# Performance work log

Hardware: AMD Instinct MI355X
Metric: run time of the kernel (lower is better)

Reference implementation:

```python
import jax, jax.numpy as jnp
import numpy as np

L, B, T, E, NH, HD, HID, V = 8, 2, 2048, 1024, 16, 64, 2816, 32000


def _rmsnorm(x, w, eps=1e-6):
    return w * (x * jax.lax.rsqrt(jnp.mean(x * x, axis=-1, keepdims=True) + eps))


def _rope(x, cos, sin):
    # x: [B,H,T,D]; cos/sin: [1,1,T,D/2]
    x1, x2 = jnp.split(x, 2, axis=-1)
    return jnp.concatenate([x1 * cos - x2 * sin, x1 * sin + x2 * cos], axis=-1)


def setup_inputs() -> dict:
    key = jax.random.key(0)
    ks = jax.random.split(key, 7)
    s = 0.02
    return {
        "idx": jax.random.randint(ks[0], (B, T), 0, V),
        "tok_emb": jax.random.normal(ks[1], (V, E), dtype=jnp.float32) * s,
        "qkv_w": jax.random.normal(ks[2], (L, 3 * E, E), dtype=jnp.float32) * s,
        "proj_w": jax.random.normal(ks[3], (L, E, E), dtype=jnp.float32) * s,
        "w1": jax.random.normal(ks[4], (L, HID, E), dtype=jnp.float32) * s,
        "w2": jax.random.normal(ks[5], (L, HID, E), dtype=jnp.float32) * s,
        "w3": jax.random.normal(ks[6], (L, E, HID), dtype=jnp.float32) * s,
        "norm1_w": jnp.ones((L, E), dtype=jnp.float32),
        "norm2_w": jnp.ones((L, E), dtype=jnp.float32),
        "norm_f_w": jnp.ones((E,), dtype=jnp.float32),
    }


def reference(idx, tok_emb, qkv_w, proj_w, w1, w2, w3, norm1_w, norm2_w, norm_f_w):
    x = tok_emb[idx]  # [B,T,E]
    # RoPE cache (start_pos=0, no kv cache -> prefill path)
    half = HD // 2
    inv_freq = 1.0 / (10000.0 ** (jnp.arange(half, dtype=jnp.float32) / half))
    pos = jnp.arange(T, dtype=jnp.float32)
    freqs = pos[:, None] * inv_freq[None, :]  # [T, D/2]
    cos = jnp.cos(freqs)[None, None]
    sin = jnp.sin(freqs)[None, None]
    causal = jnp.tril(jnp.ones((T, T), dtype=bool))
    scale = 1.0 / np.sqrt(HD).astype(np.float32)

    for l in range(L):
        # attention block
        h = _rmsnorm(x, norm1_w[l])
        qkv = h @ qkv_w[l].T  # [B,T,3E]
        q, k, v = jnp.split(qkv, 3, axis=-1)
        q = q.reshape(B, T, NH, HD).transpose(0, 2, 1, 3)
        k = k.reshape(B, T, NH, HD).transpose(0, 2, 1, 3)
        v = v.reshape(B, T, NH, HD).transpose(0, 2, 1, 3)
        q = _rope(q, cos, sin)
        k = _rope(k, cos, sin)
        att = jnp.einsum('bhqd,bhkd->bhqk', q, k) * scale
        att = jnp.where(causal, att, -jnp.inf)
        att = jax.nn.softmax(att, axis=-1)
        o = jnp.einsum('bhqk,bhkd->bhqd', att, v)
        o = o.transpose(0, 2, 1, 3).reshape(B, T, E)
        x = x + o @ proj_w[l].T
        # SwiGLU MLP
        h = _rmsnorm(x, norm2_w[l])
        x = x + (jax.nn.silu(h @ w1[l].T) * (h @ w2[l].T)) @ w3[l].T

    x = _rmsnorm(x, norm_f_w)
    logits = x @ tok_emb.T  # tied lm_head
    return logits
```

## Files before the change

### kernel.cpp

```cpp
#include <hip/hip_runtime.h>

#define GLOBAL_AS __attribute__((address_space(1)))
#define LDS_AS __attribute__((address_space(3)))

typedef unsigned short u16;
typedef unsigned int u32;
typedef __attribute__((ext_vector_type(4))) float f32x4;
typedef __attribute__((ext_vector_type(8))) short bf16x8;

#define TT 2048
#define EE 1024
#define NHH 16
#define HDD 64
#define HIDD 2816
#define VV 32000
#define MM 4096

__device__ __forceinline__ u16 f2bf(float f) {
  u32 u = __builtin_bit_cast(u32, f);
  u += 0x7fffu + ((u >> 16) & 1u);
  return (u16)(u >> 16);
}
__device__ __forceinline__ float bf2f(u16 v) {
  return __builtin_bit_cast(float, (u32)v << 16);
}


__global__ __launch_bounds__(256) void castbf_k(const float* __restrict__ in,
                                                u16* __restrict__ o, long n4) {
  const long i = (long)blockIdx.x * 256 + threadIdx.x;
  if (i >= n4) return;
  const float4 v = ((const float4*)in)[i];
  ((uint2*)o)[i] = make_uint2((u32)f2bf(v.x) | ((u32)f2bf(v.y) << 16),
                              (u32)f2bf(v.z) | ((u32)f2bf(v.w) << 16));
}

__global__ void ropetab_k(float* __restrict__ cosT, float* __restrict__ sinT) {
  const int t = blockIdx.x, j = threadIdx.x;
  const float inv = powf(10000.0f, -(float)j * (1.0f / 32.0f));
  const float f = (float)t * inv;
  cosT[t * 32 + j] = cosf(f);
  sinT[t * 32 + j] = sinf(f);
}

__global__ __launch_bounds__(256) void embed_k(const int* __restrict__ idx,
                                               const float* __restrict__ temb,
                                               float* __restrict__ x) {
  const int row = blockIdx.x;
  const int id = idx[row];
  ((float4*)(x + (size_t)row * EE))[threadIdx.x] =
      ((const float4*)(temb + (size_t)id * EE))[threadIdx.x];
}

__global__ __launch_bounds__(256) void rmsnorm_k(const float* __restrict__ x,
                                                 const float* __restrict__ w,
                                                 u16* __restrict__ o) {
  __shared__ float red[4];
  const int row = blockIdx.x, tid = threadIdx.x;
  const float4 v = ((const float4*)(x + (size_t)row * EE))[tid];
  float ss = v.x * v.x + v.y * v.y + v.z * v.z + v.w * v.w;
#pragma unroll
  for (int off = 32; off; off >>= 1) ss += __shfl_xor(ss, off, 64);
  if ((tid & 63) == 0) red[tid >> 6] = ss;
  __syncthreads();
  const float inv = rsqrtf((red[0] + red[1] + red[2] + red[3]) * (1.0f / 1024.0f) + 1e-6f);
  const float4 wv = ((const float4*)w)[tid];
  const u32 lo = (u32)f2bf(v.x * inv * wv.x) | ((u32)f2bf(v.y * inv * wv.y) << 16);
  const u32 hi = (u32)f2bf(v.z * inv * wv.z) | ((u32)f2bf(v.w * inv * wv.w) << 16);
  ((uint2*)(o + (size_t)row * EE))[tid] = make_uint2(lo, hi);
}

__global__ __launch_bounds__(512, 4) void gemm256x(const u16* __restrict__ A,
                                                   const u16* __restrict__ Bw,
                                                   float* __restrict__ C,
                                                   int N, int K) {
  __shared__ u16 lds[2 * 12288];
  const int t = threadIdx.x;
  const int lane = t & 63;
  const int w = t >> 6;
  const int wr = w >> 1;
  const int wc = w & 1;
  const int l15 = lane & 15, lg = lane >> 4;
  const int bid = blockIdx.x;
  const int row0 = (bid & 15) << 8;
  const int col0 = (bid >> 4) << 7;
  const int NT = K >> 5;

  const int gsw = (((lane & 3) ^ ((lane >> 2) & 3) ^ (lane >> 4)) << 3);
  const u16* srcA1 = A + (size_t)(row0 + (w >> 1) * 64 + (w & 1) * 16 + (lane >> 2)) * K + gsw;
  const u16* srcA2 = srcA1 + (size_t)32 * K;
  const u16* srcB = Bw + (size_t)(col0 + w * 16 + (lane >> 2)) * K + gsw;
  const int dA1 = (w >> 1) * 1024 + (w & 1) * 512 + lane * 8;
  const int dB = 8192 + w * 512 + lane * 8;

  const int usw = ((lg ^ (l15 & 3) ^ ((l15 >> 2) & 3)) << 3);
  const int abase = wr * 1024 + l15 * 32 + usw;
  const int bbase = 8192 + wc * 2048 + l15 * 32 + usw;

  f32x4 acc[4][4] = {};

  auto sA1 = [&](int kt, u16* nb) {
    __builtin_amdgcn_global_load_lds((const GLOBAL_AS void*)(srcA1 + (size_t)kt * 32),
                                     (LDS_AS void*)(nb + dA1), 16, 0, 0);
  };
  auto sA2 = [&](int kt, u16* nb) {
    __builtin_amdgcn_global_load_lds((const GLOBAL_AS void*)(srcA2 + (size_t)kt * 32),
                                     (LDS_AS void*)(nb + dA1 + 4096), 16, 0, 0);
  };
  auto sB = [&](int kt, u16* nb) {
    __builtin_amdgcn_global_load_lds((const GLOBAL_AS void*)(srcB + (size_t)kt * 32),
                                     (LDS_AS void*)(nb + dB), 16, 0, 0);
  };

  sA1(0, lds); sB(0, lds); sA2(0, lds);

  for (int kt = 0; kt < NT; ++kt) {
    const bool st = (kt + 1 < NT);
    u16* cb = lds + (kt & 1) * 12288;
    u16* nb = lds + ((kt + 1) & 1) * 12288;
    bf16x8 af[4], bfv[4];

    asm volatile("s_waitcnt vmcnt(1)" ::: "memory");
    __builtin_amdgcn_s_barrier();
#pragma unroll
    for (int mi = 0; mi < 2; ++mi) af[mi] = *(const bf16x8*)&cb[abase + mi * 512];
#pragma unroll
    for (int n = 0; n < 4; ++n) bfv[n] = *(const bf16x8*)&cb[bbase + n * 512];
    if (st) { sA1(kt + 1, nb); sB(kt + 1, nb); }
    __builtin_amdgcn_s_setprio(1);
#pragma unroll
    for (int mi = 0; mi < 2; ++mi)
#pragma unroll
      for (int n = 0; n < 4; ++n)
        acc[mi][n] = __builtin_amdgcn_mfma_f32_16x16x32_bf16(af[mi], bfv[n], acc[mi][n], 0, 0, 0);
    __builtin_amdgcn_s_setprio(0);

    if (st) { asm volatile("s_waitcnt vmcnt(2)" ::: "memory"); }
    else    { asm volatile("s_waitcnt vmcnt(0)" ::: "memory"); }
    __builtin_amdgcn_s_barrier();
#pragma unroll
    for (int mi = 0; mi < 2; ++mi) af[2 + mi] = *(const bf16x8*)&cb[abase + 4096 + mi * 512];
    if (st) sA2(kt + 1, nb);
    __builtin_amdgcn_s_setprio(1);
#pragma unroll
    for (int mi = 0; mi < 2; ++mi)
#pragma unroll
      for (int n = 0; n < 4; ++n)
        acc[2 + mi][n] = __builtin_amdgcn_mfma_f32_16x16x32_bf16(af[2 + mi], bfv[n], acc[2 + mi][n], 0, 0, 0);
    __builtin_amdgcn_s_setprio(0);
  }

#pragma unroll
  for (int m = 0; m < 4; ++m) {
    const int row = row0 + wr * 64 + m * 16 + lg * 4;
#pragma unroll
    for (int n = 0; n < 4; ++n) {
      const int col = col0 + wc * 64 + n * 16 + l15;
#pragma unroll
      for (int r = 0; r < 4; ++r)
        C[(size_t)(row + r) * N + col] = acc[m][n][r];
    }
  }
}

template <int OUTBF>
__global__ __launch_bounds__(512, 2) void gemm128n(const u16* __restrict__ A,
                                                   const u16* __restrict__ Bw,
                                                   float* __restrict__ C,
                                                   const float* __restrict__ R,
                                                   const float* __restrict__ cosT,
                                                   const float* __restrict__ sinT,
                                                   u16* __restrict__ Qb,
                                                   u16* __restrict__ Kb,
                                                   u16* __restrict__ Vtb,
                                                   int N, int K) {
  __shared__ u16 lds[4 * 8192];
  const int t = threadIdx.x;
  const int lane = t & 63;
  const int wid = t >> 6;
  const int wr = wid & 3;
  const int wc = wid >> 2;
  const int l15 = lane & 15, lg = lane >> 4;
  const int bid = blockIdx.x;
  const int row0 = (bid & 31) << 7;
  const int col0 = (bid >> 5) << 7;
  const int NT = K >> 5;

  const int rA = t >> 2;
  const int usw = (((t & 3) ^ ((t >> 3) & 3)) << 3);
  const u16* sA = A + (size_t)(row0 + rA) * K + usw;
  const u16* sB = Bw + (size_t)(col0 + rA) * K + usw;
  const int dst = t << 3;

  const int e8 = ((lg ^ ((l15 >> 1) & 3)) << 3);
  const int aoff = (wr * 32 + l15) * 32 + e8;
  const int boff = 4096 + (wc * 64 + l15) * 32 + e8;

  f32x4 acc[2][4] = {};

  auto stage = [&](int kt) {
    u16* base = &lds[(kt & 3) * 8192];
    const size_t ko = (size_t)kt * 32;
    __builtin_amdgcn_global_load_lds((const GLOBAL_AS void*)(sA + ko),
                                     (LDS_AS void*)(base + dst), 16, 0, 0);
    __builtin_amdgcn_global_load_lds((const GLOBAL_AS void*)(sB + ko),
                                     (LDS_AS void*)(base + 4096 + dst), 16, 0, 0);
  };

  stage(0);
  stage(1);
  stage(2);

  for (int kt = 0; kt < NT; ++kt) {
    const int rem = NT - 1 - kt;
    if (rem >= 2) {
      asm volatile("s_waitcnt vmcnt(4)" ::: "memory");
    } else if (rem == 1) {
      asm volatile("s_waitcnt vmcnt(2)" ::: "memory");
    } else {
      asm volatile("s_waitcnt vmcnt(0)" ::: "memory");
    }
    __builtin_amdgcn_s_barrier();
    if (kt + 3 < NT) stage(kt + 3);
    const u16* base = &lds[(kt & 3) * 8192];
    bf16x8 af[2], bfv[4];
#pragma unroll
    for (int m = 0; m < 2; ++m) af[m] = *(const bf16x8*)&base[aoff + m * 512];
#pragma unroll
    for (int n = 0; n < 4; ++n) bfv[n] = *(const bf16x8*)&base[boff + n * 512];
    __builtin_amdgcn_s_setprio(1);
#pragma unroll
    for (int m = 0; m < 2; ++m)
#pragma unroll
      for (int n = 0; n < 4; ++n)
        acc[m][n] = __builtin_amdgcn_mfma_f32_16x16x32_bf16(af[m], bfv[n], acc[m][n], 0, 0, 0);
    __builtin_amdgcn_s_setprio(0);
  }

  if (OUTBF == 3) {
    const int reg = col0 >> 10;
    const int fb = col0 & 1023;
#pragma unroll
    for (int m = 0; m < 2; ++m) {
      const int row = row0 + wr * 32 + m * 16 + lg * 4;
      const int b = row >> 11, tbase = row & 2047;
      if (reg < 2) {
        u16* dstp = (reg == 0) ? Qb : Kb;
        const float qs = (reg == 0) ? 0.18033688011112042f : 1.0f;
#pragma unroll
        for (int n = 0; n < 2; ++n) {
          const int f = fb + wc * 64 + n * 16 + l15;
          const int h = f >> 6, j = f & 63;
#pragma unroll
          for (int r = 0; r < 4; ++r) {
            const int tt = tbase + r;
            const float c = cosT[tt * 32 + j], s = sinT[tt * 32 + j];
            const float x1 = acc[m][n][r], x2 = acc[m][n | 2][r];
            const size_t ro = ((size_t)(b * NHH + h) * TT + tt) * HDD + j;
            dstp[ro] = f2bf((x1 * c - x2 * s) * qs);
            dstp[ro + 32] = f2bf((x1 * s + x2 * c) * qs);
          }
        }
      } else {
#pragma unroll
        for (int n = 0; n < 4; ++n) {
          const int f = fb + wc * 64 + n * 16 + l15;
          const int h = f >> 6, j = f & 63;
          ushort4 pk;
          pk.x = f2bf(acc[m][n][0]);
          pk.y = f2bf(acc[m][n][1]);
          pk.z = f2bf(acc[m][n][2]);
          pk.w = f2bf(acc[m][n][3]);
          *(ushort4*)&Vtb[((size_t)(b * NHH + h) * HDD + j) * TT + tbase] = pk;
        }
      }
    }
    return;
  }

#pragma unroll
  for (int m = 0; m < 2; ++m) {
    const int row = row0 + wr * 32 + m * 16 + lg * 4;
#pragma unroll
    for (int n = 0; n < 4; ++n) {
      const int col = col0 + wc * 64 + n * 16 + l15;
#pragma unroll
      for (int r = 0; r < 4; ++r) {
        const size_t o = (size_t)(row + r) * N + col;
        C[o] = acc[m][n][r] + R[o];
      }
    }
  }
}

__global__ __launch_bounds__(512, 2) void gemm128d(const u16* __restrict__ A,
                                                   const u16* __restrict__ Bg,
                                                   const u16* __restrict__ Bu,
                                                   u16* __restrict__ C16,
                                                   int N, int K) {
  __shared__ u16 lds[3 * 8192];
  const int t = threadIdx.x;
  const int lane = t & 63;
  const int wid = t >> 6;
  const int wr = wid & 3;
  const int wc = wid >> 2;
  const int l15 = lane & 15, lg = lane >> 4;
  const int bid = blockIdx.x;
  const int row0 = (bid & 31) << 7;
  const int col0 = (bid >> 5) << 6;
  const int NT = K >> 5;

  const int rA = t >> 2;
  const int usw = (((t & 3) ^ ((t >> 3) & 3)) << 3);
  const u16* sA = A + (size_t)(row0 + rA) * K + usw;
  const int tb = t & 255;
  const int rB = tb >> 2;
  const int uswB = (((tb & 3) ^ ((tb >> 3) & 3)) << 3);
  const u16* sB = ((wid < 4) ? Bg : Bu) + (size_t)(col0 + rB) * K + uswB;
  const int dstA = t << 3;
  const int dstB = 4096 + ((wid < 4) ? 0 : 2048) + (tb << 3);

  const int e8 = ((lg ^ ((l15 >> 1) & 3)) << 3);
  const int aoff = (wr * 32 + l15) * 32 + e8;
  const int goff = 4096 + (wc * 32 + l15) * 32 + e8;
  const int uoff = 6144 + (wc * 32 + l15) * 32 + e8;

  f32x4 ag[2][2] = {}, au[2][2] = {};

  auto stage = [&](int kt, int buf) {
    u16* b = &lds[buf * 8192];
    const size_t ko = (size_t)kt * 32;
    __builtin_amdgcn_global_load_lds((const GLOBAL_AS void*)(sA + ko),
                                     (LDS_AS void*)(b + dstA), 16, 0, 0);
    __builtin_amdgcn_global_load_lds((const GLOBAL_AS void*)(sB + ko),
                                     (LDS_AS void*)(b + dstB), 16, 0, 0);
  };

  stage(0, 0);
  stage(1, 1);

  int cbuf = 0;
  for (int kt = 0; kt < NT; ++kt) {
    if (kt + 1 < NT) {
      asm volatile("s_waitcnt vmcnt(2)" ::: "memory");
    } else {
      asm volatile("s_waitcnt vmcnt(0)" ::: "memory");
    }
    __builtin_amdgcn_s_barrier();
    const int nbuf = (cbuf == 2) ? 0 : cbuf + 1;
    const int sbuf = (nbuf == 2) ? 0 : nbuf + 1;
    if (kt + 2 < NT) stage(kt + 2, sbuf);
    const u16* cb = &lds[cbuf * 8192];
    bf16x8 af[2], bgv[2], buv[2];
#pragma unroll
    for (int m = 0; m < 2; ++m) af[m] = *(const bf16x8*)&cb[aoff + m * 512];
#pragma unroll
    for (int n = 0; n < 2; ++n) {
      bgv[n] = *(const bf16x8*)&cb[goff + n * 512];
      buv[n] = *(const bf16x8*)&cb[uoff + n * 512];
    }
    __builtin_amdgcn_s_setprio(1);
#pragma unroll
    for (int m = 0; m < 2; ++m)
#pragma unroll
      for (int n = 0; n < 2; ++n) {
        ag[m][n] = __builtin_amdgcn_mfma_f32_16x16x32_bf16(af[m], bgv[n], ag[m][n], 0, 0, 0);
        au[m][n] = __builtin_amdgcn_mfma_f32_16x16x32_bf16(af[m], buv[n], au[m][n], 0, 0, 0);
      }
    __builtin_amdgcn_s_setprio(0);
    cbuf = nbuf;
  }

#pragma unroll
  for (int m = 0; m < 2; ++m) {
    const int row = row0 + wr * 32 + m * 16 + lg * 4;
#pragma unroll
    for (int n = 0; n < 2; ++n) {
      const int col = col0 + wc * 32 + n * 16 + l15;
#pragma unroll
      for (int r = 0; r < 4; ++r) {
        const float g = ag[m][n][r];
        const float u = au[m][n][r];
        C16[(size_t)(row + r) * N + col] = f2bf(g / (1.0f + __expf(-g)) * u);
      }
    }
  }
}

__global__ __launch_bounds__(256) void attn_k(const u16* __restrict__ Q,
                                              const u16* __restrict__ Kc,
                                              const u16* __restrict__ Vt,
                                              u16* __restrict__ O) {
  __shared__ u16 P_lds[4][32][72];
  const int bid = blockIdx.x;
  const int bh = bid & 31;
  const int jj = bid >> 5;
  const int qi = (bid < 256) ? jj : 23 - jj;
  const int q0 = qi << 7;
  const int lane = threadIdx.x & 63;
  const int w = threadIdx.x >> 6;
  const int l15 = lane & 15, lg = lane >> 4;
  const int qbase = q0 + w * 32;

  bf16x8 qf[2][2];
#pragma unroll
  for (int am = 0; am < 2; ++am)
#pragma unroll
    for (int ks = 0; ks < 2; ++ks)
      qf[am][ks] = *(const bf16x8*)&Q[((size_t)bh * TT + qbase + am * 16 + l15) * HDD + ks * 32 + lg * 8];

  bf16x8 ones;
#pragma unroll
  for (int i = 0; i < 8; ++i) ones[i] = (short)0x3F80;

  f32x4 oacc[2][4] = {};
  f32x4 lacc[2] = {};

  const int ntile = (q0 + 128) >> 6;
  for (int kt = 0; kt < ntile; ++kt) {
    const int k0 = kt << 6;
    f32x4 s[2][4];
    bf16x8 kf0[4], kf1[4];
#pragma unroll
    for (int an = 0; an < 4; ++an) {
      kf0[an] = *(const bf16x8*)&Kc[((size_t)bh * TT + k0 + an * 16 + l15) * HDD + lg * 8];
      kf1[an] = *(const bf16x8*)&Kc[((size_t)bh * TT + k0 + an * 16 + l15) * HDD + 32 + lg * 8];
    }
    __builtin_amdgcn_s_setprio(1);
#pragma unroll
    for (int an = 0; an < 4; ++an) {
#pragma unroll
      for (int am = 0; am < 2; ++am) {
        f32x4 z = {0.0f, 0.0f, 0.0f, 0.0f};
        z = __builtin_amdgcn_mfma_f32_16x16x32_bf16(qf[am][0], kf0[an], z, 0, 0, 0);
        s[am][an] = __builtin_amdgcn_mfma_f32_16x16x32_bf16(qf[am][1], kf1[an], z, 0, 0, 0);
      }
    }
    __builtin_amdgcn_s_setprio(0);
    const bool diag = (k0 + 64) > q0;
#pragma unroll
    for (int am = 0; am < 2; ++am)
#pragma unroll
      for (int an = 0; an < 4; ++an)
#pragma unroll
        for (int r = 0; r < 4; ++r) {
          float v = s[am][an][r];
          if (diag) {
            const int qrow = qbase + am * 16 + lg * 4 + r;
            const int kcol = k0 + an * 16 + l15;
            if (kcol > qrow) v = -1e30f;
          }
          float p;
          asm("v_exp_f32 %0, %1" : "=v"(p) : "v"(v));
          s[am][an][r] = p;
        }
#pragma unroll
    for (int am = 0; am < 2; ++am)
#pragma unroll
      for (int an = 0; an < 4; ++an)
#pragma unroll
        for (int rp = 0; rp < 2; ++rp) {
          u32 pk;
          asm("v_cvt_pk_bf16_f32 %0, %1, %2"
              : "=v"(pk) : "v"(s[am][an][2 * rp]), "v"(s[am][an][2 * rp + 1]));
          const int rowb = am * 16 + lg * 4 + 2 * rp;
          P_lds[w][rowb][an * 16 + l15] = (u16)pk;
          P_lds[w][rowb + 1][an * 16 + l15] = (u16)(pk >> 16);
        }
#pragma unroll
    for (int ks = 0; ks < 2; ++ks) {
      bf16x8 pf[2];
#pragma unroll
      for (int am = 0; am < 2; ++am)
        pf[am] = *(const bf16x8*)&P_lds[w][am * 16 + l15][ks * 32 + lg * 8];
      __builtin_amdgcn_s_setprio(1);
#pragma unroll
      for (int dn = 0; dn < 4; ++dn) {
        const bf16x8 vf = *(const bf16x8*)&Vt[((size_t)bh * HDD + dn * 16 + l15) * TT + k0 + ks * 32 + lg * 8];
#pragma unroll
        for (int am = 0; am < 2; ++am)
          oacc[am][dn] = __builtin_amdgcn_mfma_f32_16x16x32_bf16(pf[am], vf, oacc[am][dn], 0, 0, 0);
      }
#pragma unroll
      for (int am = 0; am < 2; ++am)
        lacc[am] = __builtin_amdgcn_mfma_f32_16x16x32_bf16(pf[am], ones, lacc[am], 0, 0, 0);
      __builtin_amdgcn_s_setprio(0);
    }
  }
  const int b = bh >> 4, h = bh & 15;
#pragma unroll
  for (int am = 0; am < 2; ++am)
#pragma unroll
    for (int r = 0; r < 4; ++r) {
      const float il = 1.0f / lacc[am][r];
      const int qrow = qbase + am * 16 + lg * 4 + r;
#pragma unroll
      for (int dn = 0; dn < 4; ++dn)
        O[((size_t)b * TT + qrow) * EE + h * 64 + dn * 16 + l15] = f2bf(oacc[am][dn][r] * il);
    }
}


extern "C" void kernel_launch(void* const* d_in, const int* in_sizes, int n_in,
                              void* d_out, int out_size, void* d_ws, size_t ws_size,
                              hipStream_t stream) {
  const int* idx = (const int*)d_in[0];
  const float* tok_emb = (const float*)d_in[1];
  const float* qkv_w = (const float*)d_in[2];
  const float* proj_w = (const float*)d_in[3];
  const float* w1 = (const float*)d_in[4];
  const float* w2 = (const float*)d_in[5];
  const float* w3 = (const float*)d_in[6];
  const float* norm1_w = (const float*)d_in[7];
  const float* norm2_w = (const float*)d_in[8];
  const float* norm_f_w = (const float*)d_in[9];
  float* out = (float*)d_out;

  char* ws = (char*)d_ws;
  size_t off = 0;
  auto alloc = [&](size_t bytes) -> void* {
    off = (off + 255) & ~(size_t)255;
    void* p = ws + off;
    off += bytes;
    return p;
  };

  const size_t N_TEMB = (size_t)VV * EE;
  const size_t N_QKVW = (size_t)8 * 3 * EE * EE;
  const size_t N_PROJW = (size_t)8 * EE * EE;
  const size_t N_W1 = (size_t)8 * HIDD * EE;
  const size_t N_W3 = (size_t)8 * EE * HIDD;

  u16* tembbf = (u16*)alloc(N_TEMB * 2);
  u16* qkvwbf = (u16*)alloc(N_QKVW * 2);
  u16* projwbf = (u16*)alloc(N_PROJW * 2);
  u16* w1bf = (u16*)alloc(N_W1 * 2);
  u16* w2bf = (u16*)alloc(N_W1 * 2);
  u16* w3bf = (u16*)alloc(N_W3 * 2);
  float* x = (float*)alloc((size_t)MM * EE * 4);
  u16* h1 = (u16*)alloc((size_t)MM * EE * 2);
  u16* hg = (u16*)alloc((size_t)MM * HIDD * 2);
  u16* qb = (u16*)alloc((size_t)2 * NHH * TT * HDD * 2);
  u16* kb = (u16*)alloc((size_t)2 * NHH * TT * HDD * 2);
  u16* vtb = (u16*)alloc((size_t)2 * NHH * TT * HDD * 2);
  u16* attno = (u16*)alloc((size_t)MM * EE * 2);
  float* cosT = (float*)alloc((size_t)TT * 32 * 4);
  float* sinT = (float*)alloc((size_t)TT * 32 * 4);

  auto cast = [&](const float* src, u16* dst, size_t n) {
    const long n4 = (long)(n / 4);
    castbf_k<<<(int)((n4 + 255) / 256), 256, 0, stream>>>(src, dst, n4);
  };
  cast(tok_emb, tembbf, N_TEMB);
  cast(qkv_w, qkvwbf, N_QKVW);
  cast(proj_w, projwbf, N_PROJW);
  cast(w1, w1bf, N_W1);
  cast(w2, w2bf, N_W1);
  cast(w3, w3bf, N_W3);

  ropetab_k<<<TT, 32, 0, stream>>>(cosT, sinT);
  embed_k<<<MM, 256, 0, stream>>>(idx, tok_emb, x);

  for (int l = 0; l < 8; ++l) {
    rmsnorm_k<<<MM, 256, 0, stream>>>(x, norm1_w + l * EE, h1);
    gemm128n<3><<<dim3(24 * 32), 512, 0, stream>>>(h1, qkvwbf + (size_t)l * 3 * EE * EE,
                                                   nullptr, nullptr,
                                                   cosT, sinT, qb, kb, vtb, 3 * EE, EE);
    attn_k<<<dim3(512), 256, 0, stream>>>(qb, kb, vtb, attno);
    gemm128n<0><<<dim3(8 * 32), 512, 0, stream>>>(attno, projwbf + (size_t)l * EE * EE,
                                                  x, x,
                                                  nullptr, nullptr, nullptr, nullptr, nullptr,
                                                  EE, EE);
    rmsnorm_k<<<MM, 256, 0, stream>>>(x, norm2_w + l * EE, h1);
    gemm128d<<<dim3(44 * 32), 512, 0, stream>>>(h1, w1bf + (size_t)l * HIDD * EE,
                                                w2bf + (size_t)l * HIDD * EE,
                                                hg, HIDD, EE);
    gemm128n<0><<<dim3(8 * 32), 512, 0, stream>>>(hg, w3bf + (size_t)l * EE * HIDD,
                                                  x, x,
                                                  nullptr, nullptr, nullptr, nullptr, nullptr,
                                                  EE, HIDD);
  }
  rmsnorm_k<<<MM, 256, 0, stream>>>(x, norm_f_w, h1);
  gemm256x<<<dim3(250 * 16), 512, 0, stream>>>(h1, tembbf, out, VV, EE);
}
```

Measured before the change: 2.454 ms.

## Split attention across 8 waves of 16 query rows and change LM-head LDS swizzle

The attention kernel now launches 512 threads per block, with each wave owning 16 query rows instead of 32. This halves per-wave registers and MFMA work per K tile and doubles the waves available to hide latency, but each K/V fragment is now loaded by twice as many waves. Separately, the LDS swizzle pattern in the final vocab GEMM is changed, both for the global-to-LDS write offsets and the fragment read offsets, to alter the bank-conflict pattern.

```diff
diff --git a/kernel.cpp b/kernel.cpp
--- a/kernel.cpp
+++ b/kernel.cpp
@@ -86,14 +86,14 @@
   const int col0 = (bid >> 4) << 7;
   const int NT = K >> 5;
 
-  const int gsw = (((lane & 3) ^ ((lane >> 2) & 3) ^ (lane >> 4)) << 3);
+  const int gsw = (((lane & 3) ^ ((lane >> 3) & 3)) << 3);
   const u16* srcA1 = A + (size_t)(row0 + (w >> 1) * 64 + (w & 1) * 16 + (lane >> 2)) * K + gsw;
   const u16* srcA2 = srcA1 + (size_t)32 * K;
   const u16* srcB = Bw + (size_t)(col0 + w * 16 + (lane >> 2)) * K + gsw;
   const int dA1 = (w >> 1) * 1024 + (w & 1) * 512 + lane * 8;
   const int dB = 8192 + w * 512 + lane * 8;
 
-  const int usw = ((lg ^ (l15 & 3) ^ ((l15 >> 2) & 3)) << 3);
+  const int usw = ((lg ^ ((l15 >> 1) & 3)) << 3);
   const int abase = wr * 1024 + l15 * 32 + usw;
   const int bbase = 8192 + wc * 2048 + l15 * 32 + usw;
 
@@ -387,11 +387,11 @@
   }
 }
 
-__global__ __launch_bounds__(256) void attn_k(const u16* __restrict__ Q,
+__global__ __launch_bounds__(512) void attn_k(const u16* __restrict__ Q,
                                               const u16* __restrict__ Kc,
                                               const u16* __restrict__ Vt,
                                               u16* __restrict__ O) {
-  __shared__ u16 P_lds[4][32][72];
+  __shared__ u16 P_lds[8][16][72];
   const int bid = blockIdx.x;
   const int bh = bid & 31;
   const int jj = bid >> 5;
@@ -400,104 +400,80 @@
   const int lane = threadIdx.x & 63;
   const int w = threadIdx.x >> 6;
   const int l15 = lane & 15, lg = lane >> 4;
-  const int qbase = q0 + w * 32;
-
-  bf16x8 qf[2][2];
-#pragma unroll
-  for (int am = 0; am < 2; ++am)
-#pragma unroll
-    for (int ks = 0; ks < 2; ++ks)
-      qf[am][ks] = *(const bf16x8*)&Q[((size_t)bh * TT + qbase + am * 16 + l15) * HDD + ks * 32 + lg * 8];
+  const int qbase = q0 + w * 16;
+
+  bf16x8 qf[2];
+#pragma unroll
+  for (int ks = 0; ks < 2; ++ks)
+    qf[ks] = *(const bf16x8*)&Q[((size_t)bh * TT + qbase + l15) * HDD + ks * 32 + lg * 8];
 
   bf16x8 ones;
 #pragma unroll
   for (int i = 0; i < 8; ++i) ones[i] = (short)0x3F80;
 
-  f32x4 oacc[2][4] = {};
-  f32x4 lacc[2] = {};
+  f32x4 oacc[4] = {};
+  f32x4 lacc = {};
 
   const int ntile = (q0 + 128) >> 6;
   for (int kt = 0; kt < ntile; ++kt) {
     const int k0 = kt << 6;
-    f32x4 s[2][4];
-    bf16x8 kf0[4], kf1[4];
+    f32x4 s[4];
 #pragma unroll
     for (int an = 0; an < 4; ++an) {
-      kf0[an] = *(const bf16x8*)&Kc[((size_t)bh * TT + k0 + an * 16 + l15) * HDD + lg * 8];
-      kf1[an] = *(const bf16x8*)&Kc[((size_t)bh * TT + k0 + an * 16 + l15) * HDD + 32 + lg * 8];
-    }
-    __builtin_amdgcn_s_setprio(1);
-#pragma unroll
-    for (int an = 0; an < 4; ++an) {
-#pragma unroll
-      for (int am = 0; am < 2; ++am) {
-        f32x4 z = {0.0f, 0.0f, 0.0f, 0.0f};
-        z = __builtin_amdgcn_mfma_f32_16x16x32_bf16(qf[am][0], kf0[an], z, 0, 0, 0);
-        s[am][an] = __builtin_amdgcn_mfma_f32_16x16x32_bf16(qf[am][1], kf1[an], z, 0, 0, 0);
-      }
-    }
-    __builtin_amdgcn_s_setprio(0);
+      const bf16x8 kf0 = *(const bf16x8*)&Kc[((size_t)bh * TT + k0 + an * 16 + l15) * HDD + lg * 8];
+      const bf16x8 kf1 = *(const bf16x8*)&Kc[((size_t)bh * TT + k0 + an * 16 + l15) * HDD + 32 + lg * 8];
+      f32x4 z = {0.0f, 0.0f, 0.0f, 0.0f};
+      z = __builtin_amdgcn_mfma_f32_16x16x32_bf16(qf[0], kf0, z, 0, 0, 0);
+      s[an] = __builtin_amdgcn_mfma_f32_16x16x32_bf16(qf[1], kf1, z, 0, 0, 0);
+    }
     const bool diag = (k0 + 64) > q0;
 #pragma unroll
-    for (int am = 0; am < 2; ++am)
-#pragma unroll
-      for (int an = 0; an < 4; ++an)
-#pragma unroll
-        for (int r = 0; r < 4; ++r) {
-          float v = s[am][an][r];
-          if (diag) {
-            const int qrow = qbase + am * 16 + lg * 4 + r;
-            const int kcol = k0 + an * 16 + l15;
-            if (kcol > qrow) v = -1e30f;
-          }
-          float p;
-          asm("v_exp_f32 %0, %1" : "=v"(p) : "v"(v));
-          s[am][an][r] = p;
+    for (int an = 0; an < 4; ++an)
+#pragma unroll
+      for (int r = 0; r < 4; ++r) {
+        float v = s[an][r];
+        if (diag) {
+          const int qrow = qbase + lg * 4 + r;
+          const int kcol = k0 + an * 16 + l15;
+          if (kcol > qrow) v = -1e30f;
         }
-#pragma unroll
-    for (int am = 0; am < 2; ++am)
-#pragma unroll
-      for (int an = 0; an < 4; ++an)
-#pragma unroll
-        for (int rp = 0; rp < 2; ++rp) {
-          u32 pk;
-          asm("v_cvt_pk_bf16_f32 %0, %1, %2"
-              : "=v"(pk) : "v"(s[am][an][2 * rp]), "v"(s[am][an][2 * rp + 1]));
-          const int rowb = am * 16 + lg * 4 + 2 * rp;
-          P_lds[w][rowb][an * 16 + l15] = (u16)pk;
-          P_lds[w][rowb + 1][an * 16 + l15] = (u16)(pk >> 16);
-        }
+        float p;
+        asm("v_exp_f32 %0, %1" : "=v"(p) : "v"(v));
+        s[an][r] = p;
+      }
+#pragma unroll
+    for (int an = 0; an < 4; ++an)
+#pragma unroll
+      for (int rp = 0; rp < 2; ++rp) {
+        u32 pk;
+        asm("v_cvt_pk_bf16_f32 %0, %1, %2"
+            : "=v"(pk) : "v"(s[an][2 * rp]), "v"(s[an][2 * rp + 1]));
+        const int rowb = lg * 4 + 2 * rp;
+        P_lds[w][rowb][an * 16 + l15] = (u16)pk;
+        P_lds[w][rowb + 1][an * 16 + l15] = (u16)(pk >> 16);
+      }
 #pragma unroll
     for (int ks = 0; ks < 2; ++ks) {
-      bf16x8 pf[2];
-#pragma unroll
-      for (int am = 0; am < 2; ++am)
-        pf[am] = *(const bf16x8*)&P_lds[w][am * 16 + l15][ks * 32 + lg * 8];
+      const bf16x8 pf = *(const bf16x8*)&P_lds[w][l15][ks * 32 + lg * 8];
       __builtin_amdgcn_s_setprio(1);
 #pragma unroll
       for (int dn = 0; dn < 4; ++dn) {
         const bf16x8 vf = *(const bf16x8*)&Vt[((size_t)bh * HDD + dn * 16 + l15) * TT + k0 + ks * 32 + lg * 8];
-#pragma unroll
-        for (int am = 0; am < 2; ++am)
-          oacc[am][dn] = __builtin_amdgcn_mfma_f32_16x16x32_bf16(pf[am], vf, oacc[am][dn], 0, 0, 0);
-      }
-#pragma unroll
-      for (int am = 0; am < 2; ++am)
-        lacc[am] = __builtin_amdgcn_mfma_f32_16x16x32_bf16(pf[am], ones, lacc[am], 0, 0, 0);
+        oacc[dn] = __builtin_amdgcn_mfma_f32_16x16x32_bf16(pf, vf, oacc[dn], 0, 0, 0);
+      }
+      lacc = __builtin_amdgcn_mfma_f32_16x16x32_bf16(pf, ones, lacc, 0, 0, 0);
       __builtin_amdgcn_s_setprio(0);
     }
   }
   const int b = bh >> 4, h = bh & 15;
 #pragma unroll
-  for (int am = 0; am < 2; ++am)
-#pragma unroll
-    for (int r = 0; r < 4; ++r) {
-      const float il = 1.0f / lacc[am][r];
-      const int qrow = qbase + am * 16 + lg * 4 + r;
-#pragma unroll
-      for (int dn = 0; dn < 4; ++dn)
-        O[((size_t)b * TT + qrow) * EE + h * 64 + dn * 16 + l15] = f2bf(oacc[am][dn][r] * il);
-    }
+  for (int r = 0; r < 4; ++r) {
+    const float il = 1.0f / lacc[r];
+    const int qrow = qbase + lg * 4 + r;
+#pragma unroll
+    for (int dn = 0; dn < 4; ++dn)
+      O[((size_t)b * TT + qrow) * EE + h * 64 + dn * 16 + l15] = f2bf(oacc[dn][r] * il);
+  }
 }
 
 
@@ -566,7 +542,7 @@
     gemm128n<3><<<dim3(24 * 32), 512, 0, stream>>>(h1, qkvwbf + (size_t)l * 3 * EE * EE,
                                                    nullptr, nullptr,
                                                    cosT, sinT, qb, kb, vtb, 3 * EE, EE);
-    attn_k<<<dim3(512), 256, 0, stream>>>(qb, kb, vtb, attno);
+    attn_k<<<dim3(512), 512, 0, stream>>>(qb, kb, vtb, attno);
     gemm128n<0><<<dim3(8 * 32), 512, 0, stream>>>(attno, projwbf + (size_t)l * EE * EE,
                                                   x, x,
                                                   nullptr, nullptr, nullptr, nullptr, nullptr,
```

Measured after the change: 2.788 ms. 1.14x slower.
